# Performance work log

Hardware: AMD Instinct MI355X
Metric: run time of the kernel (lower is better)

## Reference

```python
import jax, jax.numpy as jnp
import numpy as np

BLOCK_SIZE = 32
# NVFP4 decode table: index bit3 = sign, bits0-2 = magnitude code
DECODE = jnp.array([0.0, 0.5, 1.0, 1.5, 2.0, 3.0, 4.0, 6.0,
                    -0.0, -0.5, -1.0, -1.5, -2.0, -3.0, -4.0, -6.0], dtype=jnp.float32)

N_OUT, K_IN = 16384, 4096


def setup_inputs() -> dict:
    key = jax.random.key(0)
    k1, k2, k3, k4 = jax.random.split(key, 4)
    x = jax.random.normal(k1, (4, 512, K_IN), dtype=jnp.float32)
    # packed uint8 stored as int32 in [0, 256)
    weight_packed = jax.random.randint(k2, (N_OUT, K_IN // 2), 0, 256, dtype=jnp.int32)
    # per-block positive scales (block_max / 6.0 in the original)
    weight_scales = jax.random.uniform(k3, (N_OUT, K_IN // BLOCK_SIZE), dtype=jnp.float32,
                                       minval=1e-3, maxval=5e-2)
    bias = jax.random.normal(k4, (N_OUT,), dtype=jnp.float32) * 0.02
    return {"x": x, "weight_packed": weight_packed, "weight_scales": weight_scales, "bias": bias}


def _dequant(weight_packed, weight_scales):
    # unpack: low nibble -> even K index, high nibble -> odd K index
    low = DECODE[weight_packed & 15]           # [N, K//2]
    high = DECODE[(weight_packed >> 4) & 15]   # [N, K//2]
    n = weight_packed.shape[0]
    w = jnp.stack([low, high], axis=-1).reshape(n, -1)  # [N, K], interleaved
    # expand per-block scales along K
    scales = jnp.repeat(weight_scales, BLOCK_SIZE, axis=1)  # [N, K]
    return w * scales


def reference(x, weight_packed, weight_scales, bias):
    w = _dequant(weight_packed, weight_scales)            # [N, K]
    out = jnp.einsum('bsk,nk->bsn', x, w) + bias          # [B, S, N]
    # activation='gelu' -> F.gelu(approximate='tanh')
    return jax.nn.gelu(out, approximate=True)
```

## Files before the change

### kernel.cpp

```cpp
#include <hip/hip_runtime.h>
#include <hip/hip_bf16.h>

typedef short bf16x8 __attribute__((ext_vector_type(8)));
typedef float f32x4 __attribute__((ext_vector_type(4)));

#define K_DIM 4096
#define N_DIM 16384
#define M_DIM 2048
#define STRIPE 16384
#define TSTRIDE (64 * STRIPE)
#define WSB_BYTES ((size_t)N_DIM * K_DIM * 2)
#define WSA_BYTES ((size_t)M_DIM * K_DIM * 2)

__device__ __forceinline__ unsigned f2bf(float f) {
    unsigned u = __builtin_bit_cast(unsigned, f);
    u += 0x7FFFu + ((u >> 16) & 1u);
    return u >> 16;
}

__device__ __forceinline__ float dec4(unsigned c, float s) {
    unsigned mag = c & 7u;
    unsigned u = (mag >= 2u) ? ((((mag >> 1) + 126u) << 23) | ((mag & 1u) << 22))
                             : (mag == 1u ? 0x3F000000u : 0u);
    u |= (c & 8u) << 28;
    return __builtin_bit_cast(float, u) * s;
}

__device__ __forceinline__ float gelu_tanh(float v) {
    float c = v + 0.044715f * v * v * v;
    float t = tanhf(0.7978845608028654f * c);
    return 0.5f * v * (1.0f + t);
}

__global__ __launch_bounds__(256) void dequant_w(const int* __restrict__ wp,
                                                 const float* __restrict__ wsc,
                                                 unsigned char* __restrict__ dst) {
    int t = blockIdx.x * 256 + threadIdx.x;
    int n = t >> 9;
    int ck = t & 511;
    int kstep = ck >> 3, s = ck & 7;
    int nt = n >> 7, r = n & 127;

    const int4 p4 = *reinterpret_cast<const int4*>(wp + (size_t)n * (K_DIM / 2) + kstep * 32 + s * 4);
    float scale = wsc[(size_t)n * (K_DIM / 32) + kstep * 2 + (s >> 2)];

    const int pv[4] = {p4.x, p4.y, p4.z, p4.w};
    unsigned o[8];
    #pragma unroll
    for (int j = 0; j < 4; ++j) {
        unsigned b = (unsigned)pv[j] & 255u;
        o[2 * j]     = f2bf(dec4(b & 15u, scale));
        o[2 * j + 1] = f2bf(dec4((b >> 4) & 15u, scale));
    }
    uint4 v;
    v.x = o[0] | (o[1] << 16);
    v.y = o[2] | (o[3] << 16);
    v.z = o[4] | (o[5] << 16);
    v.w = o[6] | (o[7] << 16);

    size_t off = (size_t)(nt * 64 + kstep) * STRIPE
               + (size_t)r * 128 + (size_t)((s ^ (r & 7)) << 4);
    *reinterpret_cast<uint4*>(dst + off) = v;
}

__global__ __launch_bounds__(256) void conv_x(const float* __restrict__ x,
                                              unsigned char* __restrict__ dst) {
    int t = blockIdx.x * 256 + threadIdx.x;
    int m = t >> 9;
    int ck = t & 511;
    int kstep = ck >> 3, s = ck & 7;
    int mt = m >> 7, r = m & 127;

    const float4* xp = reinterpret_cast<const float4*>(x + (size_t)m * K_DIM + kstep * 64 + s * 8);
    float4 a = xp[0], b = xp[1];
    uint4 v;
    v.x = f2bf(a.x) | (f2bf(a.y) << 16);
    v.y = f2bf(a.z) | (f2bf(a.w) << 16);
    v.z = f2bf(b.x) | (f2bf(b.y) << 16);
    v.w = f2bf(b.z) | (f2bf(b.w) << 16);

    size_t off = (size_t)(mt * 64 + kstep) * STRIPE
               + (size_t)r * 128 + (size_t)((s ^ (r & 7)) << 4);
    *reinterpret_cast<uint4*>(dst + off) = v;
}


__global__ __launch_bounds__(512, 2) void gemm_bf16_256(
    const unsigned char* __restrict__ wsA,
    const unsigned char* __restrict__ wsB,
    const float* __restrict__ bias,
    float* __restrict__ out)
{
    __shared__ unsigned char lds[131072];

    int id = blockIdx.x;
    int wg = (id & 7) * 64 + (id >> 3);
    int MT = wg & 7;
    int NT = wg >> 3;

    const int tid  = threadIdx.x;
    const int lane = tid & 63;
    const int w    = tid >> 6;
    const int wm   = w >> 2;
    const int wn   = w & 3;
    const int fr   = lane & 15;
    const int fg   = lane >> 4;

    const unsigned char* gA = wsA + (size_t)(2 * MT) * TSTRIDE;
    const unsigned char* gB = wsB + (size_t)(2 * NT) * TSTRIDE;

    int addrA[8];
    #pragma unroll
    for (int mi = 0; mi < 8; ++mi) {
        int row = wm * 128 + mi * 16 + fr;
        int L = row >> 1;
        addrA[mi] = L * 128 + (((((row & 1) << 2) | fg) ^ (L & 7)) << 4);
    }
    int addrB[4];
    #pragma unroll
    for (int ni = 0; ni < 4; ++ni) {
        int row = wn * 64 + ni * 16 + fr;
        int L = row >> 1;
        addrB[ni] = L * 128 + (((((row & 1) << 2) | fg) ^ (L & 7)) << 4);
    }

    int offST[2][2];
    #pragma unroll
    for (int j = 0; j < 2; ++j) {
        int c = w * 2 + j;
        int L = c * 8 + (lane >> 3);
        int p = lane & 7;
        int sl = p ^ (L & 7);
        int h = sl >> 2, fgs = sl & 3;
        int row = 2 * L + h;
        #pragma unroll
        for (int kb = 0; kb < 2; ++kb)
            offST[j][kb] = (row >> 7) * TSTRIDE + (row & 127) * 128
                         + ((((kb << 2) | fgs) ^ (row & 7)) << 4);
    }

#define GLDS(SRC, DOFF) __builtin_amdgcn_global_load_lds(                          \
        (const __attribute__((address_space(1))) unsigned int*)(SRC),              \
        (__attribute__((address_space(3))) unsigned int*)(&lds[DOFF]), 16, 0, 0)

#define STAGE_A(KSOFF, KB, SLOT) do {                                              \
        GLDS(gA + (KSOFF) + offST[0][KB], ((SLOT) << 14) + (w * 2 + 0) * 1024);    \
        GLDS(gA + (KSOFF) + offST[1][KB], ((SLOT) << 14) + (w * 2 + 1) * 1024);    \
    } while (0)
#define STAGE_B(KSOFF, KB, SLOT) do {                                              \
        GLDS(gB + (KSOFF) + offST[0][KB], 65536 + ((SLOT) << 14) + (w * 2 + 0) * 1024); \
        GLDS(gB + (KSOFF) + offST[1][KB], 65536 + ((SLOT) << 14) + (w * 2 + 1) * 1024); \
    } while (0)

#define READ_PF(PA, PB, SLOT) do {                                                 \
        const unsigned char* La_ = lds + ((SLOT) << 14);                           \
        const unsigned char* Lb_ = lds + 65536 + ((SLOT) << 14);                   \
        _Pragma("unroll") for (int ni = 0; ni < 4; ++ni)                           \
            PB[ni] = *reinterpret_cast<const bf16x8*>(Lb_ + addrB[ni]);            \
        _Pragma("unroll") for (int mi = 0; mi < 4; ++mi)                           \
            PA[mi] = *reinterpret_cast<const bf16x8*>(La_ + addrA[mi]);            \
    } while (0)

#define FENCE() do {                                                               \
        __builtin_amdgcn_sched_barrier(0);                                         \
        __builtin_amdgcn_s_barrier();                                              \
        __builtin_amdgcn_sched_barrier(0);                                         \
    } while (0)

    f32x4 acc[8][4];
    #pragma unroll
    for (int mi = 0; mi < 8; ++mi)
        #pragma unroll
        for (int ni = 0; ni < 4; ++ni)
            acc[mi][ni] = (f32x4){0.f, 0.f, 0.f, 0.f};

    bf16x8 pa0[4], pb0[4], pa1[4], pb1[4];

    STAGE_A(0, 0, 0);        STAGE_B(0, 0, 0);
    STAGE_A(0, 1, 1);        STAGE_B(0, 1, 1);
    STAGE_A(STRIPE, 0, 2);   STAGE_B(STRIPE, 0, 2);
    asm volatile("s_waitcnt vmcnt(4)" ::: "memory");
    FENCE();
    READ_PF(pa0, pb0, 0);

#define TILE_BODY(RSLOT, NSLOT, PA, PB, NPA, NPB, DO_STG, STKS, STKB, SSLOT, DO_PF, VMN) do { \
        const unsigned char* la = lds + ((RSLOT) << 14);                           \
        bf16x8 ka[4];                                                              \
        if (DO_STG) STAGE_A(STKS, STKB, SSLOT);                                    \
        _Pragma("unroll") for (int mi = 0; mi < 4; ++mi)                           \
            ka[mi] = *reinterpret_cast<const bf16x8*>(la + addrA[4 + mi]);         \
        FENCE();                                                                   \
        __builtin_amdgcn_s_setprio(1);                                             \
        _Pragma("unroll") for (int mi = 0; mi < 4; ++mi)                           \
            _Pragma("unroll") for (int ni = 0; ni < 4; ++ni)                       \
                acc[mi][ni] = __builtin_amdgcn_mfma_f32_16x16x32_bf16(             \
                    PA[mi], PB[ni], acc[mi][ni], 0, 0, 0);                         \
        __builtin_amdgcn_s_setprio(0);                                             \
        FENCE();                                                                   \
        if (DO_STG) STAGE_B(STKS, STKB, SSLOT);                                    \
        if (DO_PF) READ_PF(NPA, NPB, NSLOT);                                       \
        FENCE();                                                                   \
        __builtin_amdgcn_s_setprio(1);                                             \
        _Pragma("unroll") for (int mi = 0; mi < 4; ++mi)                           \
            _Pragma("unroll") for (int ni = 0; ni < 4; ++ni)                       \
                acc[4 + mi][ni] = __builtin_amdgcn_mfma_f32_16x16x32_bf16(         \
                    ka[mi], PB[ni], acc[4 + mi][ni], 0, 0, 0);                     \
        __builtin_amdgcn_s_setprio(0);                                             \
        if ((VMN) >= 0) {                                                          \
            if ((VMN) == 4)      asm volatile("s_waitcnt vmcnt(4)" ::: "memory");  \
            else                 asm volatile("s_waitcnt vmcnt(0)" ::: "memory");  \
            FENCE();                                                               \
        }                                                                          \
    } while (0)

    for (int tp = 0; tp < 62; ++tp) {
        const int scur = (tp & 1) << 1;
        const int ks1 = (tp + 1) * STRIPE;
        const int ks2 = (tp + 2) * STRIPE;
        TILE_BODY(scur,     scur ^ 1, pa0, pb0, pa1, pb1, 1, ks1, 1, scur ^ 3, 1, 4);
        TILE_BODY(scur ^ 1, scur ^ 2, pa1, pb1, pa0, pb0, 1, ks2, 0, scur,     1, 4);
    }
    TILE_BODY(0, 1, pa0, pb0, pa1, pb1, 1, 63 * STRIPE, 1, 3, 1, 4);
    TILE_BODY(1, 2, pa1, pb1, pa0, pb0, 0, 0, 0, 0, 1, 0);
    TILE_BODY(2, 3, pa0, pb0, pa1, pb1, 0, 0, 0, 0, 1, 0);
    TILE_BODY(3, 0, pa1, pb1, pa0, pb0, 0, 0, 0, 0, 0, -1);

    const int bm0 = MT * 256, bn0 = NT * 256;
    #pragma unroll
    for (int mi = 0; mi < 8; ++mi) {
        int row = bm0 + wm * 128 + mi * 16 + fg * 4;
        #pragma unroll
        for (int ni = 0; ni < 4; ++ni) {
            int col = bn0 + wn * 64 + ni * 16 + fr;
            float bv = bias[col];
            float* op = out + (size_t)row * N_DIM + col;
            #pragma unroll
            for (int q = 0; q < 4; ++q) {
                float v = acc[mi][ni][q] + bv;
                op[(size_t)q * N_DIM] = gelu_tanh(v);
            }
        }
    }
#undef TILE_BODY
#undef FENCE
#undef READ_PF
#undef STAGE_A
#undef STAGE_B
#undef GLDS
}

__global__ __launch_bounds__(256, 2) void nvfp4_gemm(
    const float* __restrict__ x,
    const int*   __restrict__ wp,
    const float* __restrict__ wscale,
    const float* __restrict__ bias,
    float* __restrict__ out)
{
    __shared__ uint4  lsA[128 * 8];
    __shared__ uint4  lsB[128 * 8];
    __shared__ float2 lut[256];

    const int tid = threadIdx.x;
    {
        static const float dectab[16] = {0.f, 0.5f, 1.f, 1.5f, 2.f, 3.f, 4.f, 6.f,
                                         -0.f,-0.5f,-1.f,-1.5f,-2.f,-3.f,-4.f,-6.f};
        lut[tid] = make_float2(dectab[tid & 15], dectab[(tid >> 4) & 15]);
    }

    const int bn0 = blockIdx.x * 128;
    const int bm0 = blockIdx.y * 128;
    const int r = tid >> 1;
    const int h = tid & 1;

    const float4* xp = reinterpret_cast<const float4*>(x + (size_t)(bm0 + r) * K_DIM) + h * 8;
    const uint4*  bp = reinterpret_cast<const uint4*>(wp + (size_t)(bn0 + r) * (K_DIM / 2)) + h * 4;
    const float*  sp = wscale + (size_t)(bn0 + r) * (K_DIM / 32) + h;

    float4 ax[8];
    uint4  bx[4];
    float  scale;
    #pragma unroll
    for (int j = 0; j < 8; ++j) ax[j] = xp[j];
    #pragma unroll
    for (int q = 0; q < 4; ++q) bx[q] = bp[q];
    scale = sp[0];

    f32x4 acc[4][4];
    #pragma unroll
    for (int mi = 0; mi < 4; ++mi)
        #pragma unroll
        for (int ni = 0; ni < 4; ++ni)
            acc[mi][ni] = (f32x4){0.f, 0.f, 0.f, 0.f};

    const int lane = tid & 63;
    const int wid  = tid >> 6;
    const int wm0  = (wid >> 1) * 64;
    const int wn0  = (wid & 1) * 64;
    const int fr   = lane & 15;
    const int fg   = lane >> 4;

    __syncthreads();

    for (int kt = 0; kt < 64; ++kt) {
        #pragma unroll
        for (int j = 0; j < 4; ++j) {
            float4 f0 = ax[2 * j], f1 = ax[2 * j + 1];
            uint4 v;
            v.x = f2bf(f0.x) | (f2bf(f0.y) << 16);
            v.y = f2bf(f0.z) | (f2bf(f0.w) << 16);
            v.z = f2bf(f1.x) | (f2bf(f1.y) << 16);
            v.w = f2bf(f1.z) | (f2bf(f1.w) << 16);
            lsA[(r * 8 + h * 4 + j) ^ (r & 7)] = v;
        }
        #pragma unroll
        for (int q = 0; q < 4; ++q) {
            uint4 p = bx[q];
            float2 d0 = lut[p.x & 255];
            float2 d1 = lut[p.y & 255];
            float2 d2 = lut[p.z & 255];
            float2 d3 = lut[p.w & 255];
            uint4 v;
            v.x = f2bf(d0.x * scale) | (f2bf(d0.y * scale) << 16);
            v.y = f2bf(d1.x * scale) | (f2bf(d1.y * scale) << 16);
            v.z = f2bf(d2.x * scale) | (f2bf(d2.y * scale) << 16);
            v.w = f2bf(d3.x * scale) | (f2bf(d3.y * scale) << 16);
            lsB[(r * 8 + h * 4 + q) ^ (r & 7)] = v;
        }
        __syncthreads();

        if (kt + 1 < 64) {
            #pragma unroll
            for (int j = 0; j < 8; ++j) ax[j] = xp[(kt + 1) * 16 + j];
            #pragma unroll
            for (int q = 0; q < 4; ++q) bx[q] = bp[(kt + 1) * 8 + q];
            scale = sp[(kt + 1) * 2];
        }

        #pragma unroll
        for (int kk = 0; kk < 2; ++kk) {
            bf16x8 af[4], bfr[4];
            #pragma unroll
            for (int mi = 0; mi < 4; ++mi) {
                int row = wm0 + mi * 16 + fr;
                af[mi] = __builtin_bit_cast(bf16x8, lsA[(row * 8 + kk * 4 + fg) ^ (row & 7)]);
            }
            #pragma unroll
            for (int ni = 0; ni < 4; ++ni) {
                int row = wn0 + ni * 16 + fr;
                bfr[ni] = __builtin_bit_cast(bf16x8, lsB[(row * 8 + kk * 4 + fg) ^ (row & 7)]);
            }
            #pragma unroll
            for (int mi = 0; mi < 4; ++mi)
                #pragma unroll
                for (int ni = 0; ni < 4; ++ni)
                    acc[mi][ni] = __builtin_amdgcn_mfma_f32_16x16x32_bf16(
                        af[mi], bfr[ni], acc[mi][ni], 0, 0, 0);
        }
        __syncthreads();
    }

    #pragma unroll
    for (int mi = 0; mi < 4; ++mi) {
        int row = bm0 + wm0 + mi * 16 + fg * 4;
        #pragma unroll
        for (int ni = 0; ni < 4; ++ni) {
            int col = bn0 + wn0 + ni * 16 + fr;
            float bv = bias[col];
            float* op = out + (size_t)row * N_DIM + col;
            #pragma unroll
            for (int q = 0; q < 4; ++q) {
                float v = acc[mi][ni][q] + bv;
                op[(size_t)q * N_DIM] = gelu_tanh(v);
            }
        }
    }
}

extern "C" void kernel_launch(void* const* d_in, const int* in_sizes, int n_in,
                              void* d_out, int out_size, void* d_ws, size_t ws_size,
                              hipStream_t stream) {
    const float* x    = (const float*)d_in[0];
    const int*   wp   = (const int*)d_in[1];
    const float* wsc  = (const float*)d_in[2];
    const float* bias = (const float*)d_in[3];
    float*       out  = (float*)d_out;
    (void)in_sizes; (void)n_in; (void)out_size;

    if (ws_size >= WSB_BYTES + WSA_BYTES) {
        unsigned char* wsB = (unsigned char*)d_ws;
        unsigned char* wsA = wsB + WSB_BYTES;
        dequant_w<<<(N_DIM * (K_DIM / 8)) / 256, 256, 0, stream>>>(wp, wsc, wsB);
        conv_x<<<(M_DIM * (K_DIM / 8)) / 256, 256, 0, stream>>>(x, wsA);
        gemm_bf16_256<<<(M_DIM / 256) * (N_DIM / 256), 512, 0, stream>>>(wsA, wsB, bias, out);
    } else {
        dim3 grid(N_DIM / 128, M_DIM / 128);
        nvfp4_gemm<<<grid, 256, 0, stream>>>(x, wp, wsc, bias, out);
    }
}
```

Before: 328.2 us.

## Restructure bf16 GEMM main loop into four-phase double-buffered K-tile pipeline

Replaces the two-slot register-prefetch tile body with a four-phase schedule per K-tile. Each phase loads only the A or B fragments it needs from LDS just before its MFMA block and issues one global_load_lds stage per phase. LDS is split into two double buffers, each holding two K halves. The goal is fewer live prefetch registers and a steadier spread of LDS reads and global loads across the MFMA phases. The cost is more barriers per tile and a deeper vmcnt wait, and the barrier and wait timing is hard to get right.

```diff
diff --git a/kernel.cpp b/kernel.cpp
--- a/kernel.cpp
+++ b/kernel.cpp
@@ -131,34 +131,23 @@
         int L = c * 8 + (lane >> 3);
         int p = lane & 7;
         int sl = p ^ (L & 7);
-        int h = sl >> 2, fgs = sl & 3;
+        int h = sl >> 2, kqs = sl & 3;
         int row = 2 * L + h;
         #pragma unroll
-        for (int kb = 0; kb < 2; ++kb)
-            offST[j][kb] = (row >> 7) * TSTRIDE + (row & 127) * 128
-                         + ((((kb << 2) | fgs) ^ (row & 7)) << 4);
+        for (int kk = 0; kk < 2; ++kk)
+            offST[j][kk] = (row >> 7) * TSTRIDE + (row & 127) * 128
+                         + ((((kk << 2) | kqs) ^ (row & 7)) << 4);
     }
 
 #define GLDS(SRC, DOFF) __builtin_amdgcn_global_load_lds(                          \
         (const __attribute__((address_space(1))) unsigned int*)(SRC),              \
         (__attribute__((address_space(3))) unsigned int*)(&lds[DOFF]), 16, 0, 0)
 
-#define STAGE_A(KSOFF, KB, SLOT) do {                                              \
-        GLDS(gA + (KSOFF) + offST[0][KB], ((SLOT) << 14) + (w * 2 + 0) * 1024);    \
-        GLDS(gA + (KSOFF) + offST[1][KB], ((SLOT) << 14) + (w * 2 + 1) * 1024);    \
-    } while (0)
-#define STAGE_B(KSOFF, KB, SLOT) do {                                              \
-        GLDS(gB + (KSOFF) + offST[0][KB], 65536 + ((SLOT) << 14) + (w * 2 + 0) * 1024); \
-        GLDS(gB + (KSOFF) + offST[1][KB], 65536 + ((SLOT) << 14) + (w * 2 + 1) * 1024); \
-    } while (0)
-
-#define READ_PF(PA, PB, SLOT) do {                                                 \
-        const unsigned char* La_ = lds + ((SLOT) << 14);                           \
-        const unsigned char* Lb_ = lds + 65536 + ((SLOT) << 14);                   \
-        _Pragma("unroll") for (int ni = 0; ni < 4; ++ni)                           \
-            PB[ni] = *reinterpret_cast<const bf16x8*>(Lb_ + addrB[ni]);            \
-        _Pragma("unroll") for (int mi = 0; mi < 4; ++mi)                           \
-            PA[mi] = *reinterpret_cast<const bf16x8*>(La_ + addrA[mi]);            \
+#define STG(GP, LB, KT, KK, D) do {                                                \
+        GLDS((GP) + (KT) * STRIPE + offST[0][KK],                                  \
+             (LB) + (D) * 32768 + (KK) * 16384 + (w * 2 + 0) * 1024);              \
+        GLDS((GP) + (KT) * STRIPE + offST[1][KK],                                  \
+             (LB) + (D) * 32768 + (KK) * 16384 + (w * 2 + 1) * 1024);              \
     } while (0)
 
 #define FENCE() do {                                                               \
@@ -174,56 +163,61 @@
         for (int ni = 0; ni < 4; ++ni)
             acc[mi][ni] = (f32x4){0.f, 0.f, 0.f, 0.f};
 
-    bf16x8 pa0[4], pb0[4], pa1[4], pb1[4];
-
-    STAGE_A(0, 0, 0);        STAGE_B(0, 0, 0);
-    STAGE_A(0, 1, 1);        STAGE_B(0, 1, 1);
-    STAGE_A(STRIPE, 0, 2);   STAGE_B(STRIPE, 0, 2);
-    asm volatile("s_waitcnt vmcnt(4)" ::: "memory");
-    FENCE();
-    READ_PF(pa0, pb0, 0);
-
-#define TILE_BODY(RSLOT, NSLOT, PA, PB, NPA, NPB, DO_STG, STKS, STKB, SSLOT, DO_PF, VMN) do { \
-        const unsigned char* la = lds + ((RSLOT) << 14);                           \
-        bf16x8 ka[4];                                                              \
-        if (DO_STG) STAGE_A(STKS, STKB, SSLOT);                                    \
+    bf16x8 aa[4], bb[4];
+
+#define PHASE(C, KK, MB, RDB, DOSTG, SGP, SLB, SKT, SKK, SD, VMN, ENDB) do {       \
+        const unsigned char* la_ = lds + (C) * 32768 + (KK) * 16384;               \
+        const unsigned char* lb_ = lds + 65536 + (C) * 32768 + (KK) * 16384;       \
+        if (RDB) {                                                                 \
+            _Pragma("unroll") for (int ni = 0; ni < 4; ++ni)                       \
+                bb[ni] = *reinterpret_cast<const bf16x8*>(lb_ + addrB[ni]);        \
+        }                                                                          \
         _Pragma("unroll") for (int mi = 0; mi < 4; ++mi)                           \
-            ka[mi] = *reinterpret_cast<const bf16x8*>(la + addrA[4 + mi]);         \
+            aa[mi] = *reinterpret_cast<const bf16x8*>(la_ + addrA[(MB) + mi]);     \
+        if (DOSTG) STG(SGP, SLB, SKT, SKK, SD);                                    \
         FENCE();                                                                   \
         __builtin_amdgcn_s_setprio(1);                                             \
         _Pragma("unroll") for (int mi = 0; mi < 4; ++mi)                           \
             _Pragma("unroll") for (int ni = 0; ni < 4; ++ni)                       \
-                acc[mi][ni] = __builtin_amdgcn_mfma_f32_16x16x32_bf16(             \
-                    PA[mi], PB[ni], acc[mi][ni], 0, 0, 0);                         \
+                acc[(MB) + mi][ni] = __builtin_amdgcn_mfma_f32_16x16x32_bf16(      \
+                    aa[mi], bb[ni], acc[(MB) + mi][ni], 0, 0, 0);                  \
         __builtin_amdgcn_s_setprio(0);                                             \
-        FENCE();                                                                   \
-        if (DO_STG) STAGE_B(STKS, STKB, SSLOT);                                    \
-        if (DO_PF) READ_PF(NPA, NPB, NSLOT);                                       \
-        FENCE();                                                                   \
-        __builtin_amdgcn_s_setprio(1);                                             \
-        _Pragma("unroll") for (int mi = 0; mi < 4; ++mi)                           \
-            _Pragma("unroll") for (int ni = 0; ni < 4; ++ni)                       \
-                acc[4 + mi][ni] = __builtin_amdgcn_mfma_f32_16x16x32_bf16(         \
-                    ka[mi], PB[ni], acc[4 + mi][ni], 0, 0, 0);                     \
-        __builtin_amdgcn_s_setprio(0);                                             \
-        if ((VMN) >= 0) {                                                          \
-            if ((VMN) == 4)      asm volatile("s_waitcnt vmcnt(4)" ::: "memory");  \
-            else                 asm volatile("s_waitcnt vmcnt(0)" ::: "memory");  \
-            FENCE();                                                               \
-        }                                                                          \
+        if ((VMN) == 6) { asm volatile("s_waitcnt vmcnt(6)" ::: "memory");         \
+                          __builtin_amdgcn_sched_barrier(0); }                     \
+        else if ((VMN) == 0) { asm volatile("s_waitcnt vmcnt(0)" ::: "memory");    \
+                               __builtin_amdgcn_sched_barrier(0); }                \
+        if (ENDB) FENCE();                                                         \
     } while (0)
 
-    for (int tp = 0; tp < 62; ++tp) {
-        const int scur = (tp & 1) << 1;
-        const int ks1 = (tp + 1) * STRIPE;
-        const int ks2 = (tp + 2) * STRIPE;
-        TILE_BODY(scur,     scur ^ 1, pa0, pb0, pa1, pb1, 1, ks1, 1, scur ^ 3, 1, 4);
-        TILE_BODY(scur ^ 1, scur ^ 2, pa1, pb1, pa0, pb0, 1, ks2, 0, scur,     1, 4);
-    }
-    TILE_BODY(0, 1, pa0, pb0, pa1, pb1, 1, 63 * STRIPE, 1, 3, 1, 4);
-    TILE_BODY(1, 2, pa1, pb1, pa0, pb0, 0, 0, 0, 0, 1, 0);
-    TILE_BODY(2, 3, pa0, pb0, pa1, pb1, 0, 0, 0, 0, 1, 0);
-    TILE_BODY(3, 0, pa1, pb1, pa0, pb0, 0, 0, 0, 0, 0, -1);
+#define KTILE_FULL(C, KT1, KT2) do {                                               \
+        PHASE(C, 0, 0, 1, 1, gB, 65536, KT1, 1, (C) ^ 1, -1, 1);                   \
+        PHASE(C, 0, 4, 0, 1, gA, 0,     KT2, 0, (C),     -1, 1);                   \
+        PHASE(C, 1, 0, 1, 1, gB, 65536, KT2, 0, (C),     -1, 1);                   \
+        PHASE(C, 1, 4, 0, 1, gA, 0,     KT2, 1, (C),      6, 1);                   \
+    } while (0)
+
+    STG(gA, 0,     0, 0, 0);
+    STG(gB, 65536, 0, 0, 0);
+    STG(gA, 0,     0, 1, 0);
+    STG(gB, 65536, 0, 1, 0);
+    STG(gA, 0,     1, 0, 1);
+    STG(gB, 65536, 1, 0, 1);
+    STG(gA, 0,     1, 1, 1);
+    asm volatile("s_waitcnt vmcnt(6)" ::: "memory");
+    FENCE();
+
+    for (int tp = 0; tp < 31; ++tp) {
+        KTILE_FULL(0, 2 * tp + 1, 2 * tp + 2);
+        KTILE_FULL(1, 2 * tp + 2, 2 * tp + 3);
+    }
+    PHASE(0, 0, 0, 1, 1, gB, 65536, 63, 1, 1, -1, 1);
+    PHASE(0, 0, 4, 0, 0, gA, 0, 0, 0, 0, -1, 1);
+    PHASE(0, 1, 0, 1, 0, gA, 0, 0, 0, 0, -1, 1);
+    PHASE(0, 1, 4, 0, 0, gA, 0, 0, 0, 0,  0, 1);
+    PHASE(1, 0, 0, 1, 0, gA, 0, 0, 0, 0, -1, 1);
+    PHASE(1, 0, 4, 0, 0, gA, 0, 0, 0, 0, -1, 1);
+    PHASE(1, 1, 0, 1, 0, gA, 0, 0, 0, 0, -1, 1);
+    PHASE(1, 1, 4, 0, 0, gA, 0, 0, 0, 0, -1, 0);
 
     const int bm0 = MT * 256, bn0 = NT * 256;
     #pragma unroll
@@ -241,11 +235,10 @@
             }
         }
     }
-#undef TILE_BODY
+#undef KTILE_FULL
+#undef PHASE
 #undef FENCE
-#undef READ_PF
-#undef STAGE_A
-#undef STAGE_B
+#undef STG
 #undef GLDS
 }
 
```

Result: faster. 321.2 us (-2.1%).
